# Kernel tuning notes

Hardware: AMD Instinct MI355X
Metric: run time of the kernel (lower is better)

The kernel has to match this reference:

```python
import jax, jax.numpy as jnp
import numpy as np

N = 8192
D = 512


def setup_inputs() -> dict:
    key = jax.random.key(0)
    ks = jax.random.split(key, 7)
    X = jax.random.normal(ks[0], (N, D), dtype=jnp.float32)
    adj = jax.random.randint(ks[1], (N, N), 0, 2, dtype=jnp.int32)
    # guarantee at least one neighbor per row (self-loop) so softmax is defined
    adj = adj.at[jnp.arange(N), jnp.arange(N)].set(1)
    s = 1.0 / np.sqrt(D)
    Wq = jax.random.normal(ks[2], (D, D), dtype=jnp.float32) * s
    Wk = jax.random.normal(ks[3], (D, D), dtype=jnp.float32) * s
    Wv = jax.random.normal(ks[4], (D, D), dtype=jnp.float32) * s
    Wo = jax.random.normal(ks[5], (D, D), dtype=jnp.float32) * s
    bo = jnp.zeros((D,), dtype=jnp.float32)
    return {"X": X, "adj": adj, "Wq": Wq, "Wk": Wk, "Wv": Wv, "Wo": Wo, "bo": bo}


def reference(X, adj, Wq, Wk, Wv, Wo, bo):
    # torch Linear(no bias): y = x @ W.T
    Q = X @ Wq.T                                  # [N, D]
    K = X @ Wk.T                                  # [N, D]
    V = X @ Wv.T                                  # [N, D]
    scale = 1.0 / jnp.sqrt(jnp.asarray(D, X.dtype))
    scores = jnp.einsum('nd,md->nm', Q, K) * scale  # [N, N]
    scores = jnp.where(adj == 0, -jnp.inf, scores)
    attn = jax.nn.softmax(scores, axis=-1)          # [N, N]
    out = attn @ V                                  # [N, D]
    out = out @ Wo.T + bo                           # [N, D]
    return out
```

## Files before the change

### kernel.cpp

```cpp
#include <hip/hip_runtime.h>

namespace {

constexpr int NR = 8192;
constexpr int DD = 512;
constexpr int NSPLIT = 4;
constexpr int KVLEN = NR / NSPLIT;
constexpr int KT = 32;
constexpr int NT = KVLEN / KT;
constexpr int QB = 64;
constexpr float SCALE = 0.04419417382415922f;

typedef __bf16 bf16x8 __attribute__((ext_vector_type(8)));
typedef __bf16 bf16x4 __attribute__((ext_vector_type(4)));
typedef float  f32x16 __attribute__((ext_vector_type(16)));
typedef float  f32x4  __attribute__((ext_vector_type(4)));

__device__ __forceinline__ f32x16 mfma32(bf16x8 a, bf16x8 b, f32x16 c) {
    return __builtin_amdgcn_mfma_f32_32x32x16_bf16(a, b, c, 0, 0, 0);
}
__device__ __forceinline__ f32x4 mfma16(bf16x8 a, bf16x8 b, f32x4 c) {
    return __builtin_amdgcn_mfma_f32_16x16x32_bf16(a, b, c, 0, 0, 0);
}

typedef const __attribute__((address_space(1))) void g_void;
typedef __attribute__((address_space(3))) void l_void;
__device__ __forceinline__ void lds_dma16(const void* g, void* l) {
    __builtin_amdgcn_global_load_lds((g_void*)g, (l_void*)l, 16, 0, 0);
}

__device__ __forceinline__ size_t kfa(int n, int d) {
    int tile = n >> 5, kv = n & 31;
    int chunk = (d >> 3) ^ (kv & 7);
    return (size_t)tile * 16384 + kv * 512 + chunk * 8 + (d & 7);
}
__device__ __forceinline__ size_t vfa(int n, int d) {
    size_t chunk = (size_t)(((n >> 5) * 4 + (d >> 7)) * 8 +
                            ((d >> 6) & 1) * 4 + ((d >> 5) & 1) * 2 + ((n >> 4) & 1));
    return chunk * 512 + ((((n >> 3) & 1) * 32 + (d & 31)) * 8) + (n & 7);
}

__global__ void __launch_bounds__(256)
cast_kernel(const float* __restrict__ in, __bf16* __restrict__ out, int n8) {
    int i = blockIdx.x * 256 + threadIdx.x;
    if (i >= n8) return;
    const float4* p = (const float4*)(in + (size_t)i * 8);
    float4 v0 = p[0], v1 = p[1];
    bf16x8 o;
    o[0] = (__bf16)v0.x; o[1] = (__bf16)v0.y; o[2] = (__bf16)v0.z; o[3] = (__bf16)v0.w;
    o[4] = (__bf16)v1.x; o[5] = (__bf16)v1.y; o[6] = (__bf16)v1.z; o[7] = (__bf16)v1.w;
    *(bf16x8*)(out + (size_t)i * 8) = o;
}

__global__ void __launch_bounds__(256)
bitpack_kernel(const int* __restrict__ adj, unsigned* __restrict__ abits) {
    const int w = threadIdx.x >> 6, lane = threadIdx.x & 63;
    const int q = blockIdx.x * 4 + w;
    const int* row = adj + (size_t)q * NR;
    unsigned* orow = abits + (size_t)q * 256;
    for (int i = 0; i < 128; ++i) {
        unsigned long long m = __ballot(row[i * 64 + lane] != 0);
        if (lane == 0) { orow[2 * i] = (unsigned)m; orow[2 * i + 1] = (unsigned)(m >> 32); }
    }
}

template<bool FINAL>
__global__ void __launch_bounds__(256, 2)
gemm_kernel(const __bf16* __restrict__ A, const __bf16* __restrict__ B0,
            const __bf16* __restrict__ B1, const __bf16* __restrict__ B2,
            __bf16* __restrict__ C0, __bf16* __restrict__ C1, __bf16* __restrict__ C2,
            const float* __restrict__ bias, float* __restrict__ Cf)
{
    const __bf16* B = B0;
    __bf16* Cb = C0;
    int mode = 0;
    if (!FINAL) {
        if (blockIdx.y == 1)      { B = B1; Cb = C1; mode = 1; }
        else if (blockIdx.y == 2) { B = B2; Cb = C2; }
    }
    __shared__ __bf16 As[128][72];
    __shared__ __bf16 Bs[128][72];
    const int t = threadIdx.x;
    const int w = t >> 6, lane = t & 63, lo = lane & 31, hi = lane >> 5;
    const int wm = w >> 1, wn = w & 1;
    const int bm = (blockIdx.x >> 2) * 128;
    const int bn = (blockIdx.x & 3) * 128;

    f32x16 acc[2][2];
    #pragma unroll
    for (int a = 0; a < 2; ++a)
        #pragma unroll
        for (int b = 0; b < 2; ++b)
            #pragma unroll
            for (int r = 0; r < 16; ++r) acc[a][b][r] = 0.f;

    for (int k0 = 0; k0 < DD; k0 += 64) {
        __syncthreads();
        #pragma unroll
        for (int pp = 0; pp < 2; ++pp) {
            int r = pp * 64 + (t >> 2), c = (t & 3) * 16;
            *(bf16x8*)&As[r][c]     = *(const bf16x8*)(A + (size_t)(bm + r) * DD + k0 + c);
            *(bf16x8*)&As[r][c + 8] = *(const bf16x8*)(A + (size_t)(bm + r) * DD + k0 + c + 8);
            *(bf16x8*)&Bs[r][c]     = *(const bf16x8*)(B + (size_t)(bn + r) * DD + k0 + c);
            *(bf16x8*)&Bs[r][c + 8] = *(const bf16x8*)(B + (size_t)(bn + r) * DD + k0 + c + 8);
        }
        __syncthreads();
        #pragma unroll
        for (int ks = 0; ks < 4; ++ks) {
            bf16x8 a0 = *(const bf16x8*)&As[wm * 64 + lo][ks * 16 + hi * 8];
            bf16x8 a1 = *(const bf16x8*)&As[wm * 64 + 32 + lo][ks * 16 + hi * 8];
            bf16x8 b0 = *(const bf16x8*)&Bs[wn * 64 + lo][ks * 16 + hi * 8];
            bf16x8 b1 = *(const bf16x8*)&Bs[wn * 64 + 32 + lo][ks * 16 + hi * 8];
            acc[0][0] = mfma32(a0, b0, acc[0][0]);
            acc[0][1] = mfma32(a0, b1, acc[0][1]);
            acc[1][0] = mfma32(a1, b0, acc[1][0]);
            acc[1][1] = mfma32(a1, b1, acc[1][1]);
        }
    }
    #pragma unroll
    for (int mi = 0; mi < 2; ++mi)
        #pragma unroll
        for (int ni = 0; ni < 2; ++ni) {
            int col = bn + wn * 64 + ni * 32 + lo;
            float bv = 0.f;
            if (FINAL) bv = bias[col];
            #pragma unroll
            for (int r = 0; r < 16; ++r) {
                int row = bm + wm * 64 + mi * 32 + (r & 3) + 8 * (r >> 2) + 4 * hi;
                if (FINAL) {
                    Cf[(size_t)row * DD + col] = acc[mi][ni][r] + bv;
                } else {
                    size_t a = (mode == 1) ? kfa(row, col) : ((size_t)row * DD + col);
                    Cb[a] = (__bf16)acc[mi][ni][r];
                }
            }
        }
}

__global__ void __launch_bounds__(256)
repack_v(const __bf16* __restrict__ V, __bf16* __restrict__ VF) {
    __shared__ __bf16 tile[64][72];
    const int t = threadIdx.x;
    const int rb = blockIdx.x * 64;
    const int cb = blockIdx.y * 64;
    #pragma unroll
    for (int pp = 0; pp < 2; ++pp) {
        int r = pp * 32 + (t >> 3), c = (t & 7) * 8;
        *(bf16x8*)&tile[r][c] = *(const bf16x8*)(V + (size_t)(rb + r) * DD + cb + c);
    }
    __syncthreads();
    #pragma unroll
    for (int pp = 0; pp < 2; ++pp) {
        int vid = pp * 256 + t;
        int oct = vid >> 6;
        int dd = vid & 63;
        bf16x8 o;
        #pragma unroll
        for (int e = 0; e < 8; ++e) o[e] = tile[oct * 8 + e][dd];
        *(bf16x8*)(VF + vfa(rb + oct * 8, cb + dd)) = o;
    }
}

__global__ void __launch_bounds__(256, 2)
flash_kernel(const __bf16* __restrict__ Qg, const __bf16* __restrict__ KF,
             const __bf16* __restrict__ VF, const unsigned* __restrict__ abits,
             __bf16* __restrict__ Opart, float* __restrict__ lsum_g)
{
    __shared__ __bf16 Klds[2][16384];
    __shared__ __bf16 Pl[2][QB][40];
    __shared__ float  ll[QB];

    const int t = threadIdx.x;
    const int w = t >> 6, lane = t & 63;
    const int lo = lane & 31, hi = lane >> 5;
    const int l15 = lane & 15, G = lane >> 4;
    const int bid = blockIdx.x;
    const int xcd = bid & 7;
    const int split = xcd >> 1;
    const int qblk = (((xcd & 1) << 6) | (bid >> 3)) * QB;
    const int kv0 = split * KVLEN;
    const int tile0 = kv0 >> 5;

    bf16x8 qa[16];
    #pragma unroll
    for (int ks = 0; ks < 16; ++ks)
        qa[ks] = *(const bf16x8*)(Qg + (size_t)(qblk + w * 16 + l15) * DD + ks * 32 + G * 8);

    f32x16 O[2][2][2];
    #pragma unroll
    for (int h = 0; h < 2; ++h)
        #pragma unroll
        for (int a = 0; a < 2; ++a)
            #pragma unroll
            for (int b = 0; b < 2; ++b)
                #pragma unroll
                for (int r = 0; r < 16; ++r) O[h][a][b][r] = 0.f;

    const unsigned* abp = abits + (size_t)(qblk + w * 16 + l15) * 256 + tile0;
    unsigned wcur = abp[0];
    float l_run = 0.f;
    const int hsw = l15 & 7;

    #pragma unroll
    for (int i = 0; i < 8; ++i)
        lds_dma16(KF + (size_t)tile0 * 16384 + w * 4096 + i * 512 + lane * 8,
                  &Klds[0][w * 4096 + i * 512]);
    __syncthreads();

    for (int tl = 0; tl < NT; ++tl) {
        const int b = tl & 1;
        const int tn = (tl + 1 == NT) ? 0 : tl + 1;
        #pragma unroll
        for (int i = 0; i < 8; ++i)
            lds_dma16(KF + (size_t)(tile0 + tn) * 16384 + w * 4096 + i * 512 + lane * 8,
                      &Klds[b ^ 1][w * 4096 + i * 512]);
        asm volatile("" ::: "memory");

        f32x4 St0, St1;
        #pragma unroll
        for (int r = 0; r < 4; ++r) { St0[r] = 0.f; St1[r] = 0.f; }
        #pragma unroll
        for (int ks = 0; ks < 16; ++ks) {
            int csw = (((ks * 4 + G) ^ hsw) << 3);
            bf16x8 k0 = *(const bf16x8*)&Klds[b][l15 * 512 + csw];
            bf16x8 k1 = *(const bf16x8*)&Klds[b][(16 + l15) * 512 + csw];
            St0 = mfma16(k0, qa[ks], St0);
            St1 = mfma16(k1, qa[ks], St1);
        }
        {
            float l_add = 0.f;
            bf16x4 p0v, p1v;
            #pragma unroll
            for (int r = 0; r < 4; ++r) {
                float s0 = St0[r] * SCALE;
                float s1 = St1[r] * SCALE;
                float pv0 = ((wcur >> (G * 4 + r)) & 1u) ? __expf(s0) : 0.f;
                float pv1 = ((wcur >> (16 + G * 4 + r)) & 1u) ? __expf(s1) : 0.f;
                l_add += pv0 + pv1;
                p0v[r] = (__bf16)pv0;
                p1v[r] = (__bf16)pv1;
            }
            *(bf16x4*)&Pl[b][w * 16 + l15][G * 4]      = p0v;
            *(bf16x4*)&Pl[b][w * 16 + l15][16 + G * 4] = p1v;
            float a = l_add + __shfl_xor(l_add, 16);
            a += __shfl_xor(a, 32);
            l_run += a;
        }
        unsigned wnxt = abp[tn];

        asm volatile("s_waitcnt vmcnt(1) lgkmcnt(0)" ::: "memory");
        asm volatile("s_barrier" ::: "memory");

        bf16x8 pa[2][2];
        #pragma unroll
        for (int mi = 0; mi < 2; ++mi)
            #pragma unroll
            for (int ksp = 0; ksp < 2; ++ksp)
                pa[mi][ksp] = *(const bf16x8*)&Pl[b][mi * 32 + lo][ksp * 16 + hi * 8];
        const __bf16* vf = VF + (size_t)((tile0 + tl) * 4 + w) * 4096;
        #pragma unroll
        for (int h = 0; h < 2; ++h)
            #pragma unroll
            for (int ni = 0; ni < 2; ++ni) {
                bf16x8 vb0 = *(const bf16x8*)(vf + (h * 4 + ni * 2 + 0) * 512 + lane * 8);
                bf16x8 vb1 = *(const bf16x8*)(vf + (h * 4 + ni * 2 + 1) * 512 + lane * 8);
                O[h][0][ni] = mfma32(pa[0][0], vb0, O[h][0][ni]);
                O[h][1][ni] = mfma32(pa[1][0], vb0, O[h][1][ni]);
                O[h][0][ni] = mfma32(pa[0][1], vb1, O[h][0][ni]);
                O[h][1][ni] = mfma32(pa[1][1], vb1, O[h][1][ni]);
            }
        wcur = wnxt;
    }
    if (lane < 16) {
        ll[w * 16 + lane] = l_run;
        lsum_g[(size_t)split * NR + qblk + w * 16 + lane] = l_run;
    }
    __syncthreads();
    #pragma unroll
    for (int mi = 0; mi < 2; ++mi)
        #pragma unroll
        for (int g = 0; g < 4; ++g) {
            float4 lv = *(const float4*)&ll[mi * 32 + 8 * g + 4 * hi];
            #pragma unroll
            for (int j = 0; j < 4; ++j) {
                float lval = (&lv.x)[j];
                float inv = (lval > 0.f) ? 1.f / lval : 0.f;
                int row = qblk + mi * 32 + 8 * g + 4 * hi + j;
                #pragma unroll
                for (int h = 0; h < 2; ++h)
                    #pragma unroll
                    for (int ni = 0; ni < 2; ++ni) {
                        int col = w * 128 + h * 64 + ni * 32 + lo;
                        Opart[(size_t)split * NR * DD + (size_t)row * DD + col] =
                            (__bf16)(O[h][mi][ni][g * 4 + j] * inv);
                    }
            }
        }
}

__global__ void __launch_bounds__(256)
merge_kernel(const __bf16* __restrict__ Opart, const float* __restrict__ lsum_g,
             __bf16* __restrict__ attn)
{
    int idx = blockIdx.x * 256 + threadIdx.x;
    int q = idx >> 6;
    int c = (idx & 63) * 8;
    float l0 = lsum_g[q], l1 = lsum_g[NR + q], l2 = lsum_g[2 * NR + q], l3 = lsum_g[3 * NR + q];
    float Winv = 1.f / (l0 + l1 + l2 + l3);
    float w0 = l0 * Winv, w1 = l1 * Winv, w2 = l2 * Winv, w3 = l3 * Winv;
    const size_t base = (size_t)q * DD + c;
    const size_t stride = (size_t)NR * DD;
    bf16x8 o0 = *(const bf16x8*)(Opart + base);
    bf16x8 o1 = *(const bf16x8*)(Opart + stride + base);
    bf16x8 o2 = *(const bf16x8*)(Opart + 2 * stride + base);
    bf16x8 o3 = *(const bf16x8*)(Opart + 3 * stride + base);
    bf16x8 o;
    #pragma unroll
    for (int i = 0; i < 8; ++i)
        o[i] = (__bf16)(w0 * (float)o0[i] + w1 * (float)o1[i] +
                        w2 * (float)o2[i] + w3 * (float)o3[i]);
    *(bf16x8*)(attn + base) = o;
}

}

extern "C" void kernel_launch(void* const* d_in, const int* in_sizes, int n_in,
                              void* d_out, int out_size, void* d_ws, size_t ws_size,
                              hipStream_t stream)
{
    (void)in_sizes; (void)n_in; (void)out_size; (void)ws_size;
    const float* X  = (const float*)d_in[0];
    const int*   adj = (const int*)d_in[1];
    const float* Wq = (const float*)d_in[2];
    const float* Wk = (const float*)d_in[3];
    const float* Wv = (const float*)d_in[4];
    const float* Wo = (const float*)d_in[5];
    const float* bo = (const float*)d_in[6];
    float* out = (float*)d_out;

    char* ws = (char*)d_ws;
    __bf16* Xb   = (__bf16*)(ws + 0);
    __bf16* Att  = (__bf16*)(ws + 0);
    __bf16* Wqb  = (__bf16*)(ws + 8388608);
    __bf16* Wkb  = (__bf16*)(ws + 8912896);
    __bf16* Wvb  = (__bf16*)(ws + 9437184);
    __bf16* Wob  = (__bf16*)(ws + 9961472);
    __bf16* Qb   = (__bf16*)(ws + 10485760);
    __bf16* KFb  = (__bf16*)(ws + 18874368);
    __bf16* VFb  = (__bf16*)(ws + 27262976);
    unsigned* abits = (unsigned*)(ws + 35651584);
    __bf16* Vb   = (__bf16*)(ws + 44040192);
    __bf16* Op   = (__bf16*)(ws + 44040192);
    float*  lseb = (float*)(ws + 77594624);

    bitpack_kernel<<<2048, 256, 0, stream>>>(adj, abits);
    cast_kernel<<<2048, 256, 0, stream>>>(X,  Xb,  NR * DD / 8);
    cast_kernel<<<128,  256, 0, stream>>>(Wq, Wqb, DD * DD / 8);
    cast_kernel<<<128,  256, 0, stream>>>(Wk, Wkb, DD * DD / 8);
    cast_kernel<<<128,  256, 0, stream>>>(Wv, Wvb, DD * DD / 8);
    cast_kernel<<<128,  256, 0, stream>>>(Wo, Wob, DD * DD / 8);

    gemm_kernel<false><<<dim3(256, 3), 256, 0, stream>>>(Xb, Wqb, Wkb, Wvb,
                                                         Qb, KFb, Vb, nullptr, nullptr);
    repack_v<<<dim3(128, 8), 256, 0, stream>>>(Vb, VFb);
    flash_kernel<<<512, 256, 0, stream>>>(Qb, KFb, VFb, abits, Op, lseb);
    merge_kernel<<<2048, 256, 0, stream>>>(Op, lseb, Att);
    gemm_kernel<true><<<dim3(256, 1), 256, 0, stream>>>(Att, Wob, nullptr, nullptr,
                                                        nullptr, nullptr, nullptr, bo, out);
}
```

Baseline: 443.9 us.

## Software-pipeline flash loop PV with next QK and fuse split merge into output GEMM

The flash attention loop is restructured so the P·V MFMAs for the previous tile are issued alongside the QK^T MFMAs for the current tile. V fragments and P are loaded early, and s_setprio raises wave priority during the MFMA block, which adds a prologue and an epilogue. Separately, the merge kernel is removed: the final GEMM now combines the four split partial outputs using the lsum weights while loading its A tile. This drops one launch and the write and read of the merged buffer. In exchange, the final GEMM reads the partials redundantly, once per column block.

```diff
diff --git a/kernel.cpp b/kernel.cpp
--- a/kernel.cpp
+++ b/kernel.cpp
@@ -69,7 +69,8 @@
 gemm_kernel(const __bf16* __restrict__ A, const __bf16* __restrict__ B0,
             const __bf16* __restrict__ B1, const __bf16* __restrict__ B2,
             __bf16* __restrict__ C0, __bf16* __restrict__ C1, __bf16* __restrict__ C2,
-            const float* __restrict__ bias, float* __restrict__ Cf)
+            const float* __restrict__ bias, float* __restrict__ Cf,
+            const float* __restrict__ lsum)
 {
     const __bf16* B = B0;
     __bf16* Cb = C0;
@@ -99,8 +100,31 @@
         #pragma unroll
         for (int pp = 0; pp < 2; ++pp) {
             int r = pp * 64 + (t >> 2), c = (t & 3) * 16;
-            *(bf16x8*)&As[r][c]     = *(const bf16x8*)(A + (size_t)(bm + r) * DD + k0 + c);
-            *(bf16x8*)&As[r][c + 8] = *(const bf16x8*)(A + (size_t)(bm + r) * DD + k0 + c + 8);
+            if (FINAL) {
+                int row = bm + r;
+                float l0 = lsum[row], l1 = lsum[NR + row],
+                      l2 = lsum[2 * NR + row], l3 = lsum[3 * NR + row];
+                float Winv = 1.f / (l0 + l1 + l2 + l3);
+                float w0 = l0 * Winv, w1 = l1 * Winv, w2 = l2 * Winv, w3 = l3 * Winv;
+                const size_t stride = (size_t)NR * DD;
+                #pragma unroll
+                for (int cc = 0; cc < 2; ++cc) {
+                    const size_t base = (size_t)row * DD + k0 + c + cc * 8;
+                    bf16x8 o0 = *(const bf16x8*)(A + base);
+                    bf16x8 o1 = *(const bf16x8*)(A + stride + base);
+                    bf16x8 o2 = *(const bf16x8*)(A + 2 * stride + base);
+                    bf16x8 o3 = *(const bf16x8*)(A + 3 * stride + base);
+                    bf16x8 om;
+                    #pragma unroll
+                    for (int e = 0; e < 8; ++e)
+                        om[e] = (__bf16)(w0 * (float)o0[e] + w1 * (float)o1[e] +
+                                         w2 * (float)o2[e] + w3 * (float)o3[e]);
+                    *(bf16x8*)&As[r][c + cc * 8] = om;
+                }
+            } else {
+                *(bf16x8*)&As[r][c]     = *(const bf16x8*)(A + (size_t)(bm + r) * DD + k0 + c);
+                *(bf16x8*)&As[r][c + 8] = *(const bf16x8*)(A + (size_t)(bm + r) * DD + k0 + c + 8);
+            }
             *(bf16x8*)&Bs[r][c]     = *(const bf16x8*)(B + (size_t)(bn + r) * DD + k0 + c);
             *(bf16x8*)&Bs[r][c + 8] = *(const bf16x8*)(B + (size_t)(bn + r) * DD + k0 + c + 8);
         }
@@ -205,17 +229,66 @@
     for (int i = 0; i < 8; ++i)
         lds_dma16(KF + (size_t)tile0 * 16384 + w * 4096 + i * 512 + lane * 8,
                   &Klds[0][w * 4096 + i * 512]);
+    asm volatile("s_waitcnt vmcnt(0)" ::: "memory");
     __syncthreads();
 
-    for (int tl = 0; tl < NT; ++tl) {
+    {
+        #pragma unroll
+        for (int i = 0; i < 8; ++i)
+            lds_dma16(KF + (size_t)(tile0 + 1) * 16384 + w * 4096 + i * 512 + lane * 8,
+                      &Klds[1][w * 4096 + i * 512]);
+        f32x4 St0, St1;
+        #pragma unroll
+        for (int r = 0; r < 4; ++r) { St0[r] = 0.f; St1[r] = 0.f; }
+        #pragma unroll
+        for (int ks = 0; ks < 16; ++ks) {
+            int csw = (((ks * 4 + G) ^ hsw) << 3);
+            bf16x8 k0 = *(const bf16x8*)&Klds[0][l15 * 512 + csw];
+            bf16x8 k1 = *(const bf16x8*)&Klds[0][(16 + l15) * 512 + csw];
+            St0 = mfma16(k0, qa[ks], St0);
+            St1 = mfma16(k1, qa[ks], St1);
+        }
+        float l_add = 0.f;
+        bf16x4 p0v, p1v;
+        #pragma unroll
+        for (int r = 0; r < 4; ++r) {
+            float pv0 = ((wcur >> (G * 4 + r)) & 1u) ? __expf(St0[r] * SCALE) : 0.f;
+            float pv1 = ((wcur >> (16 + G * 4 + r)) & 1u) ? __expf(St1[r] * SCALE) : 0.f;
+            l_add += pv0 + pv1;
+            p0v[r] = (__bf16)pv0; p1v[r] = (__bf16)pv1;
+        }
+        *(bf16x4*)&Pl[0][w * 16 + l15][G * 4]      = p0v;
+        *(bf16x4*)&Pl[0][w * 16 + l15][16 + G * 4] = p1v;
+        float a = l_add + __shfl_xor(l_add, 16);
+        a += __shfl_xor(a, 32);
+        l_run += a;
+        unsigned wnxt = abp[1];
+        asm volatile("s_waitcnt vmcnt(1) lgkmcnt(0)" ::: "memory");
+        asm volatile("s_barrier" ::: "memory");
+        wcur = wnxt;
+    }
+
+    for (int tl = 1; tl < NT; ++tl) {
         const int b = tl & 1;
         const int tn = (tl + 1 == NT) ? 0 : tl + 1;
+
+        const __bf16* vf = VF + (size_t)((tile0 + tl - 1) * 4 + w) * 4096;
+        bf16x8 vb[8];
+        #pragma unroll
+        for (int i = 0; i < 8; ++i)
+            vb[i] = *(const bf16x8*)(vf + i * 512 + lane * 8);
+        bf16x8 pa[2][2];
+        #pragma unroll
+        for (int mi = 0; mi < 2; ++mi)
+            #pragma unroll
+            for (int ksp = 0; ksp < 2; ++ksp)
+                pa[mi][ksp] = *(const bf16x8*)&Pl[b ^ 1][mi * 32 + lo][ksp * 16 + hi * 8];
         #pragma unroll
         for (int i = 0; i < 8; ++i)
             lds_dma16(KF + (size_t)(tile0 + tn) * 16384 + w * 4096 + i * 512 + lane * 8,
                       &Klds[b ^ 1][w * 4096 + i * 512]);
-        asm volatile("" ::: "memory");
-
+
+        __builtin_amdgcn_s_setprio(1);
         f32x4 St0, St1;
         #pragma unroll
         for (int r = 0; r < 4; ++r) { St0[r] = 0.f; St1[r] = 0.f; }
@@ -227,18 +300,26 @@
             St0 = mfma16(k0, qa[ks], St0);
             St1 = mfma16(k1, qa[ks], St1);
         }
+        #pragma unroll
+        for (int h = 0; h < 2; ++h)
+            #pragma unroll
+            for (int ni = 0; ni < 2; ++ni) {
+                O[h][0][ni] = mfma32(pa[0][0], vb[h * 4 + ni * 2 + 0], O[h][0][ni]);
+                O[h][1][ni] = mfma32(pa[1][0], vb[h * 4 + ni * 2 + 0], O[h][1][ni]);
+                O[h][0][ni] = mfma32(pa[0][1], vb[h * 4 + ni * 2 + 1], O[h][0][ni]);
+                O[h][1][ni] = mfma32(pa[1][1], vb[h * 4 + ni * 2 + 1], O[h][1][ni]);
+            }
+        __builtin_amdgcn_s_setprio(0);
+
         {
             float l_add = 0.f;
             bf16x4 p0v, p1v;
             #pragma unroll
             for (int r = 0; r < 4; ++r) {
-                float s0 = St0[r] * SCALE;
-                float s1 = St1[r] * SCALE;
-                float pv0 = ((wcur >> (G * 4 + r)) & 1u) ? __expf(s0) : 0.f;
-                float pv1 = ((wcur >> (16 + G * 4 + r)) & 1u) ? __expf(s1) : 0.f;
+                float pv0 = ((wcur >> (G * 4 + r)) & 1u) ? __expf(St0[r] * SCALE) : 0.f;
+                float pv1 = ((wcur >> (16 + G * 4 + r)) & 1u) ? __expf(St1[r] * SCALE) : 0.f;
                 l_add += pv0 + pv1;
-                p0v[r] = (__bf16)pv0;
-                p1v[r] = (__bf16)pv1;
+                p0v[r] = (__bf16)pv0; p1v[r] = (__bf16)pv1;
             }
             *(bf16x4*)&Pl[b][w * 16 + l15][G * 4]      = p0v;
             *(bf16x4*)&Pl[b][w * 16 + l15][16 + G * 4] = p1v;
@@ -247,17 +328,19 @@
             l_run += a;
         }
         unsigned wnxt = abp[tn];
-
         asm volatile("s_waitcnt vmcnt(1) lgkmcnt(0)" ::: "memory");
         asm volatile("s_barrier" ::: "memory");
-
+        wcur = wnxt;
+    }
+    {
+        const int b = (NT - 1) & 1;
         bf16x8 pa[2][2];
         #pragma unroll
         for (int mi = 0; mi < 2; ++mi)
             #pragma unroll
             for (int ksp = 0; ksp < 2; ++ksp)
                 pa[mi][ksp] = *(const bf16x8*)&Pl[b][mi * 32 + lo][ksp * 16 + hi * 8];
-        const __bf16* vf = VF + (size_t)((tile0 + tl) * 4 + w) * 4096;
+        const __bf16* vf = VF + (size_t)((tile0 + NT - 1) * 4 + w) * 4096;
         #pragma unroll
         for (int h = 0; h < 2; ++h)
             #pragma unroll
@@ -269,7 +352,6 @@
                 O[h][0][ni] = mfma32(pa[0][1], vb1, O[h][0][ni]);
                 O[h][1][ni] = mfma32(pa[1][1], vb1, O[h][1][ni]);
             }
-        wcur = wnxt;
     }
     if (lane < 16) {
         ll[w * 16 + lane] = l_run;
@@ -296,30 +378,6 @@
                     }
             }
         }
-}
-
-__global__ void __launch_bounds__(256)
-merge_kernel(const __bf16* __restrict__ Opart, const float* __restrict__ lsum_g,
-             __bf16* __restrict__ attn)
-{
-    int idx = blockIdx.x * 256 + threadIdx.x;
-    int q = idx >> 6;
-    int c = (idx & 63) * 8;
-    float l0 = lsum_g[q], l1 = lsum_g[NR + q], l2 = lsum_g[2 * NR + q], l3 = lsum_g[3 * NR + q];
-    float Winv = 1.f / (l0 + l1 + l2 + l3);
-    float w0 = l0 * Winv, w1 = l1 * Winv, w2 = l2 * Winv, w3 = l3 * Winv;
-    const size_t base = (size_t)q * DD + c;
-    const size_t stride = (size_t)NR * DD;
-    bf16x8 o0 = *(const bf16x8*)(Opart + base);
-    bf16x8 o1 = *(const bf16x8*)(Opart + stride + base);
-    bf16x8 o2 = *(const bf16x8*)(Opart + 2 * stride + base);
-    bf16x8 o3 = *(const bf16x8*)(Opart + 3 * stride + base);
-    bf16x8 o;
-    #pragma unroll
-    for (int i = 0; i < 8; ++i)
-        o[i] = (__bf16)(w0 * (float)o0[i] + w1 * (float)o1[i] +
-                        w2 * (float)o2[i] + w3 * (float)o3[i]);
-    *(bf16x8*)(attn + base) = o;
 }
 
 }
@@ -340,7 +398,6 @@
 
     char* ws = (char*)d_ws;
     __bf16* Xb   = (__bf16*)(ws + 0);
-    __bf16* Att  = (__bf16*)(ws + 0);
     __bf16* Wqb  = (__bf16*)(ws + 8388608);
     __bf16* Wkb  = (__bf16*)(ws + 8912896);
     __bf16* Wvb  = (__bf16*)(ws + 9437184);
@@ -361,10 +418,9 @@
     cast_kernel<<<128,  256, 0, stream>>>(Wo, Wob, DD * DD / 8);
 
     gemm_kernel<false><<<dim3(256, 3), 256, 0, stream>>>(Xb, Wqb, Wkb, Wvb,
-                                                         Qb, KFb, Vb, nullptr, nullptr);
+                                                         Qb, KFb, Vb, nullptr, nullptr, nullptr);
     repack_v<<<dim3(128, 8), 256, 0, stream>>>(Vb, VFb);
     flash_kernel<<<512, 256, 0, stream>>>(Qb, KFb, VFb, abits, Op, lseb);
-    merge_kernel<<<2048, 256, 0, stream>>>(Op, lseb, Att);
-    gemm_kernel<true><<<dim3(256, 1), 256, 0, stream>>>(Att, Wob, nullptr, nullptr,
-                                                        nullptr, nullptr, nullptr, bo, out);
-}
+    gemm_kernel<true><<<dim3(256, 1), 256, 0, stream>>>(Op, Wob, nullptr, nullptr,
+                                                        nullptr, nullptr, nullptr, bo, out, lseb);
+}
```

Measured after the change: 432.4 us. 2.6% less time.
